# Kernel tuning notes

Measured on AMD Instinct MI355X. Metric: run time of the kernel, lower is better.

The kernel has to match this reference:

```python
import jax, jax.numpy as jnp
import numpy as np

B, T, S, H = 4, 128, 512, 512


def setup_inputs() -> dict:
    key = jax.random.key(0)
    k1, k2, k3, k4, k5, k6, k7 = jax.random.split(key, 7)
    query = jax.random.normal(k1, (B, T, H), dtype=jnp.float32)
    encoder_outputs = jax.random.normal(k2, (B, S, H), dtype=jnp.float32)
    src_lengths = jax.random.randint(k3, (B,), 1, S + 1)
    src_lengths = src_lengths.at[0].set(S)  # torch code assumes max(len) == S
    scale = 1.0 / np.sqrt(H)
    W_h = jax.random.normal(k4, (H, H), dtype=jnp.float32) * scale
    W_s = jax.random.normal(k5, (H, H), dtype=jnp.float32) * scale
    v = jax.random.normal(k6, (H,), dtype=jnp.float32) * scale
    W_out = jax.random.normal(k7, (2 * H, H), dtype=jnp.float32) * scale
    return {"query": query, "encoder_outputs": encoder_outputs,
            "src_lengths": src_lengths, "W_h": W_h, "W_s": W_s,
            "v": v, "W_out": W_out}


def reference(query, encoder_outputs, src_lengths, W_h, W_s, v, W_out):
    # Project once, then broadcast (same math as torch's Linear on expanded tensors)
    pq = jnp.einsum('bth,hk->btk', query, W_s)            # (B,T,H) : W_s applied to query
    pe = jnp.einsum('bsh,hk->bsk', encoder_outputs, W_h)  # (B,S,H) : W_h applied to encoder
    # score(h_i, s_j) = v^T tanh(W_s q + W_h e)
    score = jnp.einsum('btsh,h->bts', jnp.tanh(pq[:, :, None, :] + pe[:, None, :, :]), v)  # (B,T,S)
    mask = (jnp.arange(score.shape[-1]) [None, :] < src_lengths[:, None])[:, None, :]  # (B,1,S)
    score = jnp.where(mask, score, -jnp.inf)
    alignment = jax.nn.softmax(score, axis=-1)            # (B,T,S)
    context = jnp.einsum('bts,bsh->bth', alignment, encoder_outputs)  # (B,T,H)
    attn_out = jnp.tanh(jnp.concatenate([context, query], axis=-1) @ W_out)  # (B,T,H)
    return attn_out
```

## Files before the change

kernel.cpp:

```cpp
#include <hip/hip_runtime.h>
#include <math.h>

#define HD 512
#define BB 4
#define TT 128
#define SS 512

typedef __attribute__((ext_vector_type(8))) short short8;
typedef __attribute__((ext_vector_type(4))) float floatx4;
typedef _Float16 half2_t __attribute__((ext_vector_type(2)));
typedef unsigned short ushort_t;
typedef unsigned int uint_t;

__device__ __forceinline__ float tanh_e(float x) {
    float t = __builtin_amdgcn_rcpf(__expf(2.f * x) + 1.f);
    return fmaf(-2.f, t, 1.f);
}
__device__ __forceinline__ ushort_t f2bf(float x) {
    unsigned int u = __float_as_uint(x);
    u += 0x7fffu + ((u >> 16) & 1u);
    return (ushort_t)(u >> 16);
}

__global__ __launch_bounds__(256) void wtrans_kernel(
    const float* __restrict__ Ws, const float* __restrict__ Wh,
    const float* __restrict__ Wo, const float* __restrict__ query,
    const float* __restrict__ enc,
    ushort_t* __restrict__ Ts, ushort_t* __restrict__ Th, ushort_t* __restrict__ To,
    ushort_t* __restrict__ cq, ushort_t* __restrict__ encB)
{
    const int bid = blockIdx.x;
    const int tid = threadIdx.x;
    if (bid < 128) {
        const float* src; ushort_t* dst; int K, l;
        if (bid < 32)      { src = Ws; dst = Ts; K = 512;  l = bid;      }
        else if (bid < 64) { src = Wh; dst = Th; K = 512;  l = bid - 32; }
        else               { src = Wo; dst = To; K = 1024; l = bid - 64; }
        const int ktiles = K >> 7;
        const int tk = l & (ktiles - 1), tn = l / ktiles;
        const int k0 = tk * 128, n0 = tn * 64;

        __shared__ ushort_t tile[64][136];

        const int lr  = tid >> 4;
        const int lc4 = (tid & 15) * 4;
        #pragma unroll
        for (int p = 0; p < 8; ++p) {
            const int row = p * 16 + lr;
            float4 s = *(const float4*)(src + (size_t)(k0 + row) * HD + n0 + lc4);
            tile[lc4 + 0][row] = f2bf(s.x);
            tile[lc4 + 1][row] = f2bf(s.y);
            tile[lc4 + 2][row] = f2bf(s.z);
            tile[lc4 + 3][row] = f2bf(s.w);
        }
        __syncthreads();
        const int n = tid >> 2, kc = (tid & 3) * 32;
        #pragma unroll
        for (int j = 0; j < 4; ++j) {
            uint4 o = *(const uint4*)&tile[n][kc + j * 8];
            *(uint4*)&dst[(size_t)(n0 + n) * K + k0 + kc + j * 8] = o;
        }
    } else if (bid < 256) {
        const int idx = ((bid - 128) * 256 + tid) * 8;
        const int m = idx >> 9, h = idx & 511;
        float4 q0 = *(const float4*)(query + (size_t)m * HD + h);
        float4 q1 = *(const float4*)(query + (size_t)m * HD + h + 4);
        uint4 o;
        o.x = (uint_t)f2bf(q0.x) | ((uint_t)f2bf(q0.y) << 16);
        o.y = (uint_t)f2bf(q0.z) | ((uint_t)f2bf(q0.w) << 16);
        o.z = (uint_t)f2bf(q1.x) | ((uint_t)f2bf(q1.y) << 16);
        o.w = (uint_t)f2bf(q1.z) | ((uint_t)f2bf(q1.w) << 16);
        *(uint4*)&cq[(size_t)m * 1024 + 512 + h] = o;
    } else {
        const size_t idx = ((size_t)(bid - 256) * 256 + tid) * 8;
        float4 e0 = *(const float4*)(enc + idx);
        float4 e1 = *(const float4*)(enc + idx + 4);
        uint4 o;
        o.x = (uint_t)f2bf(e0.x) | ((uint_t)f2bf(e0.y) << 16);
        o.y = (uint_t)f2bf(e0.z) | ((uint_t)f2bf(e0.w) << 16);
        o.z = (uint_t)f2bf(e1.x) | ((uint_t)f2bf(e1.y) << 16);
        o.w = (uint_t)f2bf(e1.z) | ((uint_t)f2bf(e1.w) << 16);
        *(uint4*)&encB[idx] = o;
    }
}

#define LDP 40
__global__ __launch_bounds__(256) void proj_kernel(
    const ushort_t* __restrict__ cq, const ushort_t* __restrict__ encB,
    const ushort_t* __restrict__ WTs, const ushort_t* __restrict__ WTh,
    const ushort_t* __restrict__ WTo, const float* __restrict__ v,
    float2* __restrict__ tqa, _Float16* __restrict__ peT,
    _Float16* __restrict__ encWo, float* __restrict__ qWob)
{
    const int bm = blockIdx.x;
    const int bn = blockIdx.y;
    int type; const ushort_t* A; int lda; const ushort_t* B; int ldb; int m0;
    if (bm < 8)       { type = 0; A = cq + 512; lda = 1024; B = WTs;       ldb = 512;  m0 = bm * 64;        }
    else if (bm < 40) { type = 1; A = encB;     lda = 512;  B = WTh;       ldb = 512;  m0 = (bm - 8) * 64;  }
    else if (bm < 72) { type = 2; A = encB;     lda = 512;  B = WTo;       ldb = 1024; m0 = (bm - 40) * 64; }
    else              { type = 3; A = cq + 512; lda = 1024; B = WTo + 512; ldb = 1024; m0 = (bm - 72) * 64; }
    const int n0 = bn * 64;

    __shared__ ushort_t As[64 * LDP];
    __shared__ ushort_t Bs[64 * LDP];

    const int tid = threadIdx.x;
    const int lane = tid & 63, w = tid >> 6;
    const int quad = lane >> 4, lrow = lane & 15;
    const int mw = (w & 1) * 32, nw = (w >> 1) * 32;

    const int ar = tid >> 2;
    const int ac = (tid & 3) * 8;

    floatx4 zero = {0.f, 0.f, 0.f, 0.f};
    floatx4 acc[2][2] = {{zero, zero}, {zero, zero}};

    uint4 ald = *(const uint4*)&A[(size_t)(m0 + ar) * lda + ac];
    uint4 bld = *(const uint4*)&B[(size_t)(n0 + ar) * ldb + ac];

    for (int k0 = 0; k0 < HD; k0 += 32) {
        __syncthreads();
        *(uint4*)&As[ar * LDP + ac] = ald;
        *(uint4*)&Bs[ar * LDP + ac] = bld;
        __syncthreads();
        if (k0 + 32 < HD) {
            ald = *(const uint4*)&A[(size_t)(m0 + ar) * lda + k0 + 32 + ac];
            bld = *(const uint4*)&B[(size_t)(n0 + ar) * ldb + k0 + 32 + ac];
        }
        short8 af[2], bf[2];
        #pragma unroll
        for (int i = 0; i < 2; ++i)
            af[i] = *(const short8*)&As[(mw + i * 16 + lrow) * LDP + quad * 8];
        #pragma unroll
        for (int j = 0; j < 2; ++j)
            bf[j] = *(const short8*)&Bs[(nw + j * 16 + lrow) * LDP + quad * 8];
        #pragma unroll
        for (int i = 0; i < 2; ++i)
            #pragma unroll
            for (int j = 0; j < 2; ++j)
                acc[i][j] = __builtin_amdgcn_mfma_f32_16x16x32_bf16(af[i], bf[j], acc[i][j], 0, 0, 0);
    }

    if (type == 0) {
        #pragma unroll
        for (int j = 0; j < 2; ++j) {
            const int col = n0 + nw + j * 16 + lrow;
            const float vj = v[col];
            #pragma unroll
            for (int i = 0; i < 2; ++i)
                #pragma unroll
                for (int r = 0; r < 4; ++r) {
                    const int row = m0 + mw + i * 16 + quad * 4 + r;
                    float tq = tanh_e(acc[i][j][r]);
                    float2 o; o.x = tq; o.y = vj * tq;
                    tqa[(size_t)row * HD + col] = o;
                }
        }
    } else if (type == 1) {
        #pragma unroll
        for (int i = 0; i < 2; ++i)
            #pragma unroll
            for (int j = 0; j < 2; ++j) {
                const int gm = m0 + mw + i * 16 + quad * 4;
                const int b = gm >> 9, s = gm & 511;
                const int col = n0 + nw + j * 16 + lrow;
                _Float16 t0 = (_Float16)tanh_e(acc[i][j][0]);
                _Float16 t1 = (_Float16)tanh_e(acc[i][j][1]);
                _Float16 t2 = (_Float16)tanh_e(acc[i][j][2]);
                _Float16 t3 = (_Float16)tanh_e(acc[i][j][3]);
                ushort4 o;
                o.x = *(ushort_t*)&t0; o.y = *(ushort_t*)&t1;
                o.z = *(ushort_t*)&t2; o.w = *(ushort_t*)&t3;
                *(ushort4*)((ushort_t*)peT + ((size_t)b * HD + col) * SS + s) = o;
            }
    } else if (type == 2) {
        #pragma unroll
        for (int i = 0; i < 2; ++i)
            #pragma unroll
            for (int j = 0; j < 2; ++j) {
                const int col = n0 + nw + j * 16 + lrow;
                #pragma unroll
                for (int r = 0; r < 4; ++r) {
                    const int gm = m0 + mw + i * 16 + quad * 4 + r;
                    encWo[(size_t)gm * HD + col] = (_Float16)acc[i][j][r];
                }
            }
    } else {
        #pragma unroll
        for (int i = 0; i < 2; ++i)
            #pragma unroll
            for (int j = 0; j < 2; ++j) {
                const int col = n0 + nw + j * 16 + lrow;
                #pragma unroll
                for (int r = 0; r < 4; ++r) {
                    const int gm = m0 + mw + i * 16 + quad * 4 + r;
                    qWob[(size_t)gm * HD + col] = acc[i][j][r];
                }
            }
    }
}

__global__ __launch_bounds__(1024, 8) void fused_kernel(
    const float2* __restrict__ tqa, const _Float16* __restrict__ peT,
    const float* __restrict__ vv, const _Float16* __restrict__ encWo,
    const float* __restrict__ qWob, const int* __restrict__ lens,
    float* __restrict__ out)
{
    const int bt = blockIdx.x;
    const int b = bt >> 7;
    const int tid = threadIdx.x;
    const int lane = tid & 63, wid = tid >> 6;
    const int len = lens[b];

    __shared__ uint4  s_tab[HD];
    __shared__ float  s_part[7 * SS];
    __shared__ float  s_sc[SS];
    __shared__ uint_t s_al2[SS];
    __shared__ float  s_red[32];

    if (tid < HD) {
        float2 q = tqa[(size_t)bt * HD + tid];
        float vh = vv[tid];
        _Float16 tqh = (_Float16)q.x, vvh = (_Float16)vh, vth = (_Float16)q.y;
        uint_t ta = *(ushort_t*)&tqh, tb = *(ushort_t*)&vvh, tc = *(ushort_t*)&vth;
        uint4 e4; e4.x = ta | (ta << 16); e4.y = tb | (tb << 16); e4.z = tc | (tc << 16); e4.w = 0;
        s_tab[tid] = e4;
    }
    __syncthreads();

    const int sg = tid & 127, hq = tid >> 7;
    const int s0 = sg * 4;
    const int hbase = hq * 64;
    float a0 = 0.f, a1 = 0.f, a2 = 0.f, a3 = 0.f;
    if (s0 < len) {
        const ushort_t* colp = (const ushort_t*)peT + ((size_t)b * HD + hbase) * SS + s0;
        const uint4* tabp = &s_tab[hbase];
        half2_t one2; one2[0] = (_Float16)1.f; one2[1] = (_Float16)1.f;
        #pragma unroll 2
        for (int i = 0; i < 32; ++i) {
            uint2 pA = *(const uint2*)(colp);
            uint2 pB = *(const uint2*)(colp + SS);
            colp += 2 * SS;
            uint4 cA = tabp[2 * i], cB = tabp[2 * i + 1];
            half2_t tqA = *(half2_t*)&cA.x, vA = *(half2_t*)&cA.y, vtA = *(half2_t*)&cA.z;
            half2_t tqB = *(half2_t*)&cB.x, vB = *(half2_t*)&cB.y, vtB = *(half2_t*)&cB.z;
            half2_t teA01 = *(half2_t*)&pA.x, teA23 = *(half2_t*)&pA.y;
            half2_t teB01 = *(half2_t*)&pB.x, teB23 = *(half2_t*)&pB.y;
            half2_t dA01 = tqA * teA01 + one2, dA23 = tqA * teA23 + one2;
            half2_t dB01 = tqB * teB01 + one2, dB23 = tqB * teB23 + one2;
            half2_t mA01 = vA * teA01 + vtA,  mA23 = vA * teA23 + vtA;
            half2_t mB01 = vB * teB01 + vtB,  mB23 = vB * teB23 + vtB;
            half2_t n01 = mA01 * dB01 + mB01 * dA01;
            half2_t n23 = mA23 * dB23 + mB23 * dA23;
            half2_t d01 = dA01 * dB01, d23 = dA23 * dB23;
            a0 = fmaf((float)n01[0], __builtin_amdgcn_rcpf((float)d01[0]), a0);
            a1 = fmaf((float)n01[1], __builtin_amdgcn_rcpf((float)d01[1]), a1);
            a2 = fmaf((float)n23[0], __builtin_amdgcn_rcpf((float)d23[0]), a2);
            a3 = fmaf((float)n23[1], __builtin_amdgcn_rcpf((float)d23[1]), a3);
        }
    }
    if (hq) {
        float4 p; p.x = a0; p.y = a1; p.z = a2; p.w = a3;
        *(float4*)&s_part[(hq - 1) * SS + s0] = p;
    }
    __syncthreads();
    if (!hq) {
        float t0 = a0, t1 = a1, t2 = a2, t3 = a3;
        #pragma unroll
        for (int q = 0; q < 7; ++q) {
            float4 p = *(const float4*)&s_part[q * SS + s0];
            t0 += p.x; t1 += p.y; t2 += p.z; t3 += p.w;
        }
        s_sc[s0]     = (s0     < len) ? t0 : -INFINITY;
        s_sc[s0 + 1] = (s0 + 1 < len) ? t1 : -INFINITY;
        s_sc[s0 + 2] = (s0 + 2 < len) ? t2 : -INFINITY;
        s_sc[s0 + 3] = (s0 + 3 < len) ? t3 : -INFINITY;
    }
    __syncthreads();

    float sc = (tid < SS) ? s_sc[tid] : -INFINITY;
    float m = sc;
    #pragma unroll
    for (int off = 32; off; off >>= 1) m = fmaxf(m, __shfl_xor(m, off, 64));
    if (lane == 0) s_red[wid] = m;
    __syncthreads();
    m = s_red[0];
    #pragma unroll
    for (int i2 = 1; i2 < 16; ++i2) m = fmaxf(m, s_red[i2]);

    float e = (tid < SS) ? __expf(sc - m) : 0.f;
    float sum = e;
    #pragma unroll
    for (int off = 32; off; off >>= 1) sum += __shfl_xor(sum, off, 64);
    if (lane == 0) s_red[16 + wid] = sum;
    __syncthreads();
    float total = s_red[16];
    #pragma unroll
    for (int i2 = 1; i2 < 16; ++i2) total += s_red[16 + i2];
    if (tid < SS) {
        float a = e * __builtin_amdgcn_rcpf(total);
        _Float16 ah = (_Float16)a;
        uint_t ap = *(ushort_t*)&ah;
        s_al2[tid] = ap | (ap << 16);
    }
    __syncthreads();

    const int ng = tid & 127, sq = tid >> 7;
    const int n0 = ng * 4;
    const int sbeg = sq * 64;
    float o0 = 0.f, o1 = 0.f, o2 = 0.f, o3 = 0.f;
    {
        const ushort_t* ew = (const ushort_t*)encWo + ((size_t)b * SS + sbeg) * HD + n0;
        const int rem = (len > sbeg) ? ((len - sbeg < 64) ? len - sbeg : 64) : 0;
        const int schunks = (rem + 7) >> 3;
        for (int c = 0; c < schunks; ++c) {
            half2_t acc01; acc01[0] = (_Float16)0.f; acc01[1] = (_Float16)0.f;
            half2_t acc23; acc23[0] = (_Float16)0.f; acc23[1] = (_Float16)0.f;
            const ushort_t* ewc = ew + (size_t)(c * 8) * HD;
            #pragma unroll
            for (int k = 0; k < 8; ++k) {
                uint2 wv = *(const uint2*)(ewc + (size_t)k * HD);
                uint_t av = s_al2[sbeg + c * 8 + k];
                half2_t a2h = *(half2_t*)&av;
                acc01 = a2h * (*(half2_t*)&wv.x) + acc01;
                acc23 = a2h * (*(half2_t*)&wv.y) + acc23;
            }
            o0 += (float)acc01[0]; o1 += (float)acc01[1];
            o2 += (float)acc23[0]; o3 += (float)acc23[1];
        }
    }
    if (sq) {
        float4 p; p.x = o0; p.y = o1; p.z = o2; p.w = o3;
        *(float4*)&s_part[(sq - 1) * SS + n0] = p;
    }
    __syncthreads();
    if (!sq) {
        #pragma unroll
        for (int q = 0; q < 7; ++q) {
            float4 p = *(const float4*)&s_part[q * SS + n0];
            o0 += p.x; o1 += p.y; o2 += p.z; o3 += p.w;
        }
        float4 qb = *(const float4*)(qWob + (size_t)bt * HD + n0);
        float4 ov;
        ov.x = tanh_e(o0 + qb.x); ov.y = tanh_e(o1 + qb.y);
        ov.z = tanh_e(o2 + qb.z); ov.w = tanh_e(o3 + qb.w);
        *(float4*)(out + (size_t)bt * HD + n0) = ov;
    }
}

extern "C" void kernel_launch(void* const* d_in, const int* in_sizes, int n_in,
                              void* d_out, int out_size, void* d_ws, size_t ws_size,
                              hipStream_t stream) {
    (void)in_sizes; (void)n_in; (void)out_size; (void)ws_size;
    const float* query = (const float*)d_in[0];
    const float* enc   = (const float*)d_in[1];
    const int*   lens  = (const int*)d_in[2];
    const float* W_h   = (const float*)d_in[3];
    const float* W_s   = (const float*)d_in[4];
    const float* v     = (const float*)d_in[5];
    const float* W_out = (const float*)d_in[6];
    float* out = (float*)d_out;

    ushort_t* WTs   = (ushort_t*)d_ws;
    ushort_t* WTh   = WTs + (size_t)HD * HD;
    ushort_t* WTo   = WTh + (size_t)HD * HD;
    ushort_t* encB  = WTo + (size_t)HD * 2 * HD;
    float2*   tqa   = (float2*)(encB + (size_t)BB * SS * HD);
    _Float16* peT   = (_Float16*)(tqa + (size_t)BB * TT * HD);
    _Float16* encWo = peT + (size_t)BB * HD * SS;
    float*    qWob  = (float*)(encWo + (size_t)BB * SS * HD);
    ushort_t* cq    = (ushort_t*)(qWob + (size_t)BB * TT * HD);

    wtrans_kernel<<<dim3(768), 256, 0, stream>>>(W_s, W_h, W_out, query, enc,
                                                 WTs, WTh, WTo, cq, encB);
    proj_kernel<<<dim3(80, 8), 256, 0, stream>>>(cq, encB, WTs, WTh, WTo, v,
                                                 tqa, peT, encWo, qWob);
    fused_kernel<<<dim3(BB * TT), 1024, 0, stream>>>(tqa, peT, v, encWo, qWob, lens, out);
}
```

Baseline: 118.2 us.

## Process two query timesteps per block to reuse encoder loads

Each fused block now handles two consecutive query rows, so every peT and encWo element loaded from global memory feeds two score or context computations instead of one. The score loop widens to 8 sources per thread and splits H across 16 waves, and partial sums are reduced across all waves through a larger shared buffer. This halves the grid to 256 blocks and raises shared memory and register use, which may lower occupancy and leave some CUs idle.

```diff
diff --git a/kernel.cpp b/kernel.cpp
--- a/kernel.cpp
+++ b/kernel.cpp
@@ -200,151 +200,200 @@
     }
 }
 
-__global__ __launch_bounds__(1024, 8) void fused_kernel(
+__global__ __launch_bounds__(1024, 4) void fused_kernel(
     const float2* __restrict__ tqa, const _Float16* __restrict__ peT,
     const float* __restrict__ vv, const _Float16* __restrict__ encWo,
     const float* __restrict__ qWob, const int* __restrict__ lens,
     float* __restrict__ out)
 {
-    const int bt = blockIdx.x;
-    const int b = bt >> 7;
+    const int bt0 = blockIdx.x * 2;
+    const int b = bt0 >> 7;
     const int tid = threadIdx.x;
     const int lane = tid & 63, wid = tid >> 6;
     const int len = lens[b];
 
-    __shared__ uint4  s_tab[HD];
-    __shared__ float  s_part[7 * SS];
-    __shared__ float  s_sc[SS];
-    __shared__ uint_t s_al2[SS];
+    __shared__ uint4  s_tab[2][HD];
+    __shared__ float  s_part[16][2][SS];
+    __shared__ float  s_sc[2][SS];
+    __shared__ uint_t s_al2[SS][2];
     __shared__ float  s_red[32];
 
-    if (tid < HD) {
-        float2 q = tqa[(size_t)bt * HD + tid];
-        float vh = vv[tid];
+    {
+        const int t_loc = tid >> 9, h = tid & 511;
+        float2 q = tqa[(size_t)(bt0 + t_loc) * HD + h];
+        float vh = vv[h];
         _Float16 tqh = (_Float16)q.x, vvh = (_Float16)vh, vth = (_Float16)q.y;
         uint_t ta = *(ushort_t*)&tqh, tb = *(ushort_t*)&vvh, tc = *(ushort_t*)&vth;
         uint4 e4; e4.x = ta | (ta << 16); e4.y = tb | (tb << 16); e4.z = tc | (tc << 16); e4.w = 0;
-        s_tab[tid] = e4;
-    }
-    __syncthreads();
-
-    const int sg = tid & 127, hq = tid >> 7;
-    const int s0 = sg * 4;
-    const int hbase = hq * 64;
-    float a0 = 0.f, a1 = 0.f, a2 = 0.f, a3 = 0.f;
+        s_tab[t_loc][h] = e4;
+    }
+    __syncthreads();
+
+    const int sg = tid & 63;
+    const int hq = (tid >> 6) & 7, sub = tid >> 9;
+    const int s0 = sg * 8;
+    const int hbase = hq * 64 + sub * 32;
+    float p0[8] = {0.f,0.f,0.f,0.f,0.f,0.f,0.f,0.f};
+    float p1[8] = {0.f,0.f,0.f,0.f,0.f,0.f,0.f,0.f};
     if (s0 < len) {
         const ushort_t* colp = (const ushort_t*)peT + ((size_t)b * HD + hbase) * SS + s0;
-        const uint4* tabp = &s_tab[hbase];
+        const uint4* tp0 = &s_tab[0][hbase];
+        const uint4* tp1 = &s_tab[1][hbase];
         half2_t one2; one2[0] = (_Float16)1.f; one2[1] = (_Float16)1.f;
         #pragma unroll 2
-        for (int i = 0; i < 32; ++i) {
-            uint2 pA = *(const uint2*)(colp);
-            uint2 pB = *(const uint2*)(colp + SS);
+        for (int i = 0; i < 16; ++i) {
+            uint4 pA = *(const uint4*)(colp);
+            uint4 pB = *(const uint4*)(colp + SS);
             colp += 2 * SS;
-            uint4 cA = tabp[2 * i], cB = tabp[2 * i + 1];
-            half2_t tqA = *(half2_t*)&cA.x, vA = *(half2_t*)&cA.y, vtA = *(half2_t*)&cA.z;
-            half2_t tqB = *(half2_t*)&cB.x, vB = *(half2_t*)&cB.y, vtB = *(half2_t*)&cB.z;
-            half2_t teA01 = *(half2_t*)&pA.x, teA23 = *(half2_t*)&pA.y;
-            half2_t teB01 = *(half2_t*)&pB.x, teB23 = *(half2_t*)&pB.y;
-            half2_t dA01 = tqA * teA01 + one2, dA23 = tqA * teA23 + one2;
-            half2_t dB01 = tqB * teB01 + one2, dB23 = tqB * teB23 + one2;
-            half2_t mA01 = vA * teA01 + vtA,  mA23 = vA * teA23 + vtA;
-            half2_t mB01 = vB * teB01 + vtB,  mB23 = vB * teB23 + vtB;
-            half2_t n01 = mA01 * dB01 + mB01 * dA01;
-            half2_t n23 = mA23 * dB23 + mB23 * dA23;
-            half2_t d01 = dA01 * dB01, d23 = dA23 * dB23;
-            a0 = fmaf((float)n01[0], __builtin_amdgcn_rcpf((float)d01[0]), a0);
-            a1 = fmaf((float)n01[1], __builtin_amdgcn_rcpf((float)d01[1]), a1);
-            a2 = fmaf((float)n23[0], __builtin_amdgcn_rcpf((float)d23[0]), a2);
-            a3 = fmaf((float)n23[1], __builtin_amdgcn_rcpf((float)d23[1]), a3);
-        }
-    }
-    if (hq) {
-        float4 p; p.x = a0; p.y = a1; p.z = a2; p.w = a3;
-        *(float4*)&s_part[(hq - 1) * SS + s0] = p;
-    }
-    __syncthreads();
-    if (!hq) {
-        float t0 = a0, t1 = a1, t2 = a2, t3 = a3;
-        #pragma unroll
-        for (int q = 0; q < 7; ++q) {
-            float4 p = *(const float4*)&s_part[q * SS + s0];
-            t0 += p.x; t1 += p.y; t2 += p.z; t3 += p.w;
-        }
-        s_sc[s0]     = (s0     < len) ? t0 : -INFINITY;
-        s_sc[s0 + 1] = (s0 + 1 < len) ? t1 : -INFINITY;
-        s_sc[s0 + 2] = (s0 + 2 < len) ? t2 : -INFINITY;
-        s_sc[s0 + 3] = (s0 + 3 < len) ? t3 : -INFINITY;
-    }
-    __syncthreads();
-
-    float sc = (tid < SS) ? s_sc[tid] : -INFINITY;
-    float m = sc;
-    #pragma unroll
-    for (int off = 32; off; off >>= 1) m = fmaxf(m, __shfl_xor(m, off, 64));
-    if (lane == 0) s_red[wid] = m;
-    __syncthreads();
-    m = s_red[0];
-    #pragma unroll
-    for (int i2 = 1; i2 < 16; ++i2) m = fmaxf(m, s_red[i2]);
-
-    float e = (tid < SS) ? __expf(sc - m) : 0.f;
-    float sum = e;
-    #pragma unroll
-    for (int off = 32; off; off >>= 1) sum += __shfl_xor(sum, off, 64);
-    if (lane == 0) s_red[16 + wid] = sum;
-    __syncthreads();
-    float total = s_red[16];
-    #pragma unroll
-    for (int i2 = 1; i2 < 16; ++i2) total += s_red[16 + i2];
-    if (tid < SS) {
+            uint4 cA0 = tp0[2 * i], cB0 = tp0[2 * i + 1];
+            uint4 cA1 = tp1[2 * i], cB1 = tp1[2 * i + 1];
+            half2_t teA0 = *(half2_t*)&pA.x, teA1 = *(half2_t*)&pA.y;
+            half2_t teA2 = *(half2_t*)&pA.z, teA3 = *(half2_t*)&pA.w;
+            half2_t teB0 = *(half2_t*)&pB.x, teB1 = *(half2_t*)&pB.y;
+            half2_t teB2 = *(half2_t*)&pB.z, teB3 = *(half2_t*)&pB.w;
+            {
+                half2_t tqA = *(half2_t*)&cA0.x, vA = *(half2_t*)&cA0.y, vtA = *(half2_t*)&cA0.z;
+                half2_t tqB = *(half2_t*)&cB0.x, vB = *(half2_t*)&cB0.y, vtB = *(half2_t*)&cB0.z;
+                half2_t dA0 = tqA * teA0 + one2, dA1 = tqA * teA1 + one2;
+                half2_t dA2 = tqA * teA2 + one2, dA3 = tqA * teA3 + one2;
+                half2_t dB0 = tqB * teB0 + one2, dB1 = tqB * teB1 + one2;
+                half2_t dB2 = tqB * teB2 + one2, dB3 = tqB * teB3 + one2;
+                half2_t mA0 = vA * teA0 + vtA, mA1 = vA * teA1 + vtA;
+                half2_t mA2 = vA * teA2 + vtA, mA3 = vA * teA3 + vtA;
+                half2_t mB0 = vB * teB0 + vtB, mB1 = vB * teB1 + vtB;
+                half2_t mB2 = vB * teB2 + vtB, mB3 = vB * teB3 + vtB;
+                half2_t n0h = mA0 * dB0 + mB0 * dA0, n1h = mA1 * dB1 + mB1 * dA1;
+                half2_t n2h = mA2 * dB2 + mB2 * dA2, n3h = mA3 * dB3 + mB3 * dA3;
+                half2_t d0h = dA0 * dB0, d1h = dA1 * dB1;
+                half2_t d2h = dA2 * dB2, d3h = dA3 * dB3;
+                p0[0] = fmaf((float)n0h[0], __builtin_amdgcn_rcpf((float)d0h[0]), p0[0]);
+                p0[1] = fmaf((float)n0h[1], __builtin_amdgcn_rcpf((float)d0h[1]), p0[1]);
+                p0[2] = fmaf((float)n1h[0], __builtin_amdgcn_rcpf((float)d1h[0]), p0[2]);
+                p0[3] = fmaf((float)n1h[1], __builtin_amdgcn_rcpf((float)d1h[1]), p0[3]);
+                p0[4] = fmaf((float)n2h[0], __builtin_amdgcn_rcpf((float)d2h[0]), p0[4]);
+                p0[5] = fmaf((float)n2h[1], __builtin_amdgcn_rcpf((float)d2h[1]), p0[5]);
+                p0[6] = fmaf((float)n3h[0], __builtin_amdgcn_rcpf((float)d3h[0]), p0[6]);
+                p0[7] = fmaf((float)n3h[1], __builtin_amdgcn_rcpf((float)d3h[1]), p0[7]);
+            }
+            {
+                half2_t tqA = *(half2_t*)&cA1.x, vA = *(half2_t*)&cA1.y, vtA = *(half2_t*)&cA1.z;
+                half2_t tqB = *(half2_t*)&cB1.x, vB = *(half2_t*)&cB1.y, vtB = *(half2_t*)&cB1.z;
+                half2_t dA0 = tqA * teA0 + one2, dA1 = tqA * teA1 + one2;
+                half2_t dA2 = tqA * teA2 + one2, dA3 = tqA * teA3 + one2;
+                half2_t dB0 = tqB * teB0 + one2, dB1 = tqB * teB1 + one2;
+                half2_t dB2 = tqB * teB2 + one2, dB3 = tqB * teB3 + one2;
+                half2_t mA0 = vA * teA0 + vtA, mA1 = vA * teA1 + vtA;
+                half2_t mA2 = vA * teA2 + vtA, mA3 = vA * teA3 + vtA;
+                half2_t mB0 = vB * teB0 + vtB, mB1 = vB * teB1 + vtB;
+                half2_t mB2 = vB * teB2 + vtB, mB3 = vB * teB3 + vtB;
+                half2_t n0h = mA0 * dB0 + mB0 * dA0, n1h = mA1 * dB1 + mB1 * dA1;
+                half2_t n2h = mA2 * dB2 + mB2 * dA2, n3h = mA3 * dB3 + mB3 * dA3;
+                half2_t d0h = dA0 * dB0, d1h = dA1 * dB1;
+                half2_t d2h = dA2 * dB2, d3h = dA3 * dB3;
+                p1[0] = fmaf((float)n0h[0], __builtin_amdgcn_rcpf((float)d0h[0]), p1[0]);
+                p1[1] = fmaf((float)n0h[1], __builtin_amdgcn_rcpf((float)d0h[1]), p1[1]);
+                p1[2] = fmaf((float)n1h[0], __builtin_amdgcn_rcpf((float)d1h[0]), p1[2]);
+                p1[3] = fmaf((float)n1h[1], __builtin_amdgcn_rcpf((float)d1h[1]), p1[3]);
+                p1[4] = fmaf((float)n2h[0], __builtin_amdgcn_rcpf((float)d2h[0]), p1[4]);
+                p1[5] = fmaf((float)n2h[1], __builtin_amdgcn_rcpf((float)d2h[1]), p1[5]);
+                p1[6] = fmaf((float)n3h[0], __builtin_amdgcn_rcpf((float)d3h[0]), p1[6]);
+                p1[7] = fmaf((float)n3h[1], __builtin_amdgcn_rcpf((float)d3h[1]), p1[7]);
+            }
+        }
+    }
+    {
+        float4 w0; w0.x = p0[0]; w0.y = p0[1]; w0.z = p0[2]; w0.w = p0[3];
+        float4 w1; w1.x = p0[4]; w1.y = p0[5]; w1.z = p0[6]; w1.w = p0[7];
+        *(float4*)&s_part[wid][0][s0]     = w0;
+        *(float4*)&s_part[wid][0][s0 + 4] = w1;
+        float4 w2; w2.x = p1[0]; w2.y = p1[1]; w2.z = p1[2]; w2.w = p1[3];
+        float4 w3; w3.x = p1[4]; w3.y = p1[5]; w3.z = p1[6]; w3.w = p1[7];
+        *(float4*)&s_part[wid][1][s0]     = w2;
+        *(float4*)&s_part[wid][1][s0 + 4] = w3;
+    }
+    __syncthreads();
+    {
+        const int t_loc = tid >> 9, s = tid & 511;
+        float acc = 0.f;
+        #pragma unroll
+        for (int q = 0; q < 16; ++q) acc += s_part[q][t_loc][s];
+        s_sc[t_loc][s] = (s < len) ? acc : -INFINITY;
+    }
+    __syncthreads();
+
+    {
+        const int t_loc = tid >> 9;
+        float sc = s_sc[t_loc][tid & 511];
+        float m = sc;
+        #pragma unroll
+        for (int off = 32; off; off >>= 1) m = fmaxf(m, __shfl_xor(m, off, 64));
+        if (lane == 0) s_red[wid] = m;
+        __syncthreads();
+        const int rb = (t_loc << 3);
+        m = s_red[rb];
+        #pragma unroll
+        for (int i2 = 1; i2 < 8; ++i2) m = fmaxf(m, s_red[rb + i2]);
+
+        float e = __expf(sc - m);
+        float sum = e;
+        #pragma unroll
+        for (int off = 32; off; off >>= 1) sum += __shfl_xor(sum, off, 64);
+        if (lane == 0) s_red[16 + wid] = sum;
+        __syncthreads();
+        float total = s_red[16 + rb];
+        #pragma unroll
+        for (int i2 = 1; i2 < 8; ++i2) total += s_red[16 + rb + i2];
         float a = e * __builtin_amdgcn_rcpf(total);
         _Float16 ah = (_Float16)a;
         uint_t ap = *(ushort_t*)&ah;
-        s_al2[tid] = ap | (ap << 16);
+        s_al2[tid & 511][t_loc] = ap | (ap << 16);
     }
     __syncthreads();
 
     const int ng = tid & 127, sq = tid >> 7;
     const int n0 = ng * 4;
     const int sbeg = sq * 64;
-    float o0 = 0.f, o1 = 0.f, o2 = 0.f, o3 = 0.f;
+    float fo0[4] = {0.f, 0.f, 0.f, 0.f};
+    float fo1[4] = {0.f, 0.f, 0.f, 0.f};
     {
         const ushort_t* ew = (const ushort_t*)encWo + ((size_t)b * SS + sbeg) * HD + n0;
         const int rem = (len > sbeg) ? ((len - sbeg < 64) ? len - sbeg : 64) : 0;
         const int schunks = (rem + 7) >> 3;
         for (int c = 0; c < schunks; ++c) {
-            half2_t acc01; acc01[0] = (_Float16)0.f; acc01[1] = (_Float16)0.f;
-            half2_t acc23; acc23[0] = (_Float16)0.f; acc23[1] = (_Float16)0.f;
+            half2_t a01_0, a23_0, a01_1, a23_1;
+            a01_0[0] = (_Float16)0.f; a01_0[1] = (_Float16)0.f;
+            a23_0 = a01_0; a01_1 = a01_0; a23_1 = a01_0;
             const ushort_t* ewc = ew + (size_t)(c * 8) * HD;
             #pragma unroll
             for (int k = 0; k < 8; ++k) {
                 uint2 wv = *(const uint2*)(ewc + (size_t)k * HD);
-                uint_t av = s_al2[sbeg + c * 8 + k];
-                half2_t a2h = *(half2_t*)&av;
-                acc01 = a2h * (*(half2_t*)&wv.x) + acc01;
-                acc23 = a2h * (*(half2_t*)&wv.y) + acc23;
-            }
-            o0 += (float)acc01[0]; o1 += (float)acc01[1];
-            o2 += (float)acc23[0]; o3 += (float)acc23[1];
-        }
-    }
-    if (sq) {
-        float4 p; p.x = o0; p.y = o1; p.z = o2; p.w = o3;
-        *(float4*)&s_part[(sq - 1) * SS + n0] = p;
-    }
-    __syncthreads();
-    if (!sq) {
-        #pragma unroll
-        for (int q = 0; q < 7; ++q) {
-            float4 p = *(const float4*)&s_part[q * SS + n0];
-            o0 += p.x; o1 += p.y; o2 += p.z; o3 += p.w;
-        }
-        float4 qb = *(const float4*)(qWob + (size_t)bt * HD + n0);
-        float4 ov;
-        ov.x = tanh_e(o0 + qb.x); ov.y = tanh_e(o1 + qb.y);
-        ov.z = tanh_e(o2 + qb.z); ov.w = tanh_e(o3 + qb.w);
-        *(float4*)(out + (size_t)bt * HD + n0) = ov;
+                uint2 av = *(const uint2*)&s_al2[sbeg + c * 8 + k][0];
+                half2_t w01 = *(half2_t*)&wv.x, w23 = *(half2_t*)&wv.y;
+                half2_t al0 = *(half2_t*)&av.x, al1 = *(half2_t*)&av.y;
+                a01_0 = al0 * w01 + a01_0; a23_0 = al0 * w23 + a23_0;
+                a01_1 = al1 * w01 + a01_1; a23_1 = al1 * w23 + a23_1;
+            }
+            fo0[0] += (float)a01_0[0]; fo0[1] += (float)a01_0[1];
+            fo0[2] += (float)a23_0[0]; fo0[3] += (float)a23_0[1];
+            fo1[0] += (float)a01_1[0]; fo1[1] += (float)a01_1[1];
+            fo1[2] += (float)a23_1[0]; fo1[3] += (float)a23_1[1];
+        }
+    }
+    __syncthreads();
+    {
+        float4 w0; w0.x = fo0[0]; w0.y = fo0[1]; w0.z = fo0[2]; w0.w = fo0[3];
+        float4 w1; w1.x = fo1[0]; w1.y = fo1[1]; w1.z = fo1[2]; w1.w = fo1[3];
+        *(float4*)&s_part[sq][0][n0] = w0;
+        *(float4*)&s_part[sq][1][n0] = w1;
+    }
+    __syncthreads();
+    {
+        const int t_loc = tid >> 9, n = tid & 511;
+        float acc = 0.f;
+        #pragma unroll
+        for (int q = 0; q < 8; ++q) acc += s_part[q][t_loc][n];
+        acc += qWob[(size_t)(bt0 + t_loc) * HD + n];
+        out[(size_t)(bt0 + t_loc) * HD + n] = tanh_e(acc);
     }
 }
 
@@ -375,5 +424,5 @@
                                                  WTs, WTh, WTo, cq, encB);
     proj_kernel<<<dim3(80, 8), 256, 0, stream>>>(cq, encB, WTs, WTh, WTo, v,
                                                  tqa, peT, encWo, qWob);
-    fused_kernel<<<dim3(BB * TT), 1024, 0, stream>>>(tqa, peT, v, encWo, qWob, lens, out);
-}
+    fused_kernel<<<dim3(BB * TT / 2), 1024, 0, stream>>>(tqa, peT, v, encWo, qWob, lens, out);
+}
```

After: 112.5 us. 1.05x faster.
